# Performance work log

Measured on AMD Instinct MI355X. Metric: run time of the kernel, lower is better.

## Reference

```python
import jax, jax.numpy as jnp
import numpy as np

N, E = 100000, 640000
H, EDGE_D, ATOM_D, RD, L = 128, 10, 25, 64, 4


def _gelu(t):
    return jax.nn.gelu(t, approximate=True)  # tanh approximation, matches torch GELU(approximate='tanh')


def _mlp2(t, w1, b1, w2, b2):
    return _gelu(t @ w1 + b1) @ w2 + b2


def setup_inputs() -> dict:
    key = jax.random.key(0)
    ks = iter(jax.random.split(key, 64))
    s = 0.05
    d = {}
    d['x'] = jax.random.normal(next(ks), (N, ATOM_D), jnp.float32)
    d['edge_index'] = jax.random.randint(next(ks), (2, E), 0, N, jnp.int32)
    d['edge_attr'] = jax.random.normal(next(ks), (E, EDGE_D), jnp.float32)
    d['enc_w1'] = jax.random.normal(next(ks), (ATOM_D, H)) * s
    d['enc_b1'] = jnp.zeros((H,))
    d['enc_w2'] = jax.random.normal(next(ks), (H, H)) * s
    d['enc_b2'] = jnp.zeros((H,))
    d['edge_w1'] = jax.random.normal(next(ks), (L, EDGE_D, H)) * s
    d['edge_b1'] = jnp.zeros((L, H))
    d['edge_w2'] = jax.random.normal(next(ks), (L, H, H)) * s
    d['edge_b2'] = jnp.zeros((L, H))
    d['msg_w1'] = jax.random.normal(next(ks), (L, H, H)) * s
    d['msg_b1'] = jnp.zeros((L, H))
    d['msg_w2'] = jax.random.normal(next(ks), (L, H, H)) * s
    d['msg_b2'] = jnp.zeros((L, H))
    d['gate_w'] = jax.random.normal(next(ks), (L, 2 * H, H)) * s
    d['gate_b'] = jnp.zeros((L, H))
    d['ln_g'] = jnp.ones((L, H))
    d['ln_b'] = jnp.zeros((L, H))
    for name in ('ion', 'pka', 'acid'):
        d[name + '_w1'] = jax.random.normal(next(ks), (H, RD)) * s
        d[name + '_b1'] = jnp.zeros((RD,))
        d[name + '_w2'] = jax.random.normal(next(ks), (RD, 1)) * s
        d[name + '_b2'] = jnp.zeros((1,))
    return d


def reference(x, edge_index, edge_attr, enc_w1, enc_b1, enc_w2, enc_b2,
              edge_w1, edge_b1, edge_w2, edge_b2,
              msg_w1, msg_b1, msg_w2, msg_b2,
              gate_w, gate_b, ln_g, ln_b,
              ion_w1, ion_b1, ion_w2, ion_b2,
              pka_w1, pka_b1, pka_w2, pka_b2,
              acid_w1, acid_b1, acid_w2, acid_b2):
    src, dst = edge_index[0], edge_index[1]
    n = x.shape[0]
    h = _mlp2(x, enc_w1, enc_b1, enc_w2, enc_b2)  # [N, H]
    ones_e = jnp.ones((src.shape[0],), x.dtype)
    count = jnp.clip(jax.ops.segment_sum(ones_e, dst, num_segments=n), 1.0)[:, None]  # [N,1]
    for i in range(L):
        ew = _mlp2(edge_attr, edge_w1[i], edge_b1[i], edge_w2[i], edge_b2[i])  # [E, H]
        msg = _mlp2(h[src], msg_w1[i], msg_b1[i], msg_w2[i], msg_b2[i]) * ew   # [E, H]
        agg = jax.ops.segment_sum(msg, dst, num_segments=n) / count           # [N, H] mean agg
        gate = jax.nn.sigmoid(jnp.concatenate([h, agg], axis=-1) @ gate_w[i] + gate_b[i])
        h = h + gate * agg
        mu = jnp.mean(h, axis=-1, keepdims=True)
        var = jnp.mean(jnp.square(h - mu), axis=-1, keepdims=True)
        h = (h - mu) * jax.lax.rsqrt(var + 1e-5) * ln_g[i] + ln_b[i]
    ion = _mlp2(h, ion_w1, ion_b1, ion_w2, ion_b2)
    pka = _mlp2(h, pka_w1, pka_b1, pka_w2, pka_b2)
    acid = _mlp2(h, acid_w1, acid_b1, acid_w2, acid_b2)
    return (ion, pka, acid)
```

## Files before the change

### kernel.cpp

```cpp
#include <hip/hip_runtime.h>
#include <math.h>

#define NN 100000
#define NN2 100032
#define NE 640000
#define H 128
#define AD 25
#define ED 10
#define RD 64
#define NL 4
#define NB_E (NE / 64 + 1)
#define NSB ((NN + 255) / 256)
#define CAP 256

typedef short bfrag __attribute__((ext_vector_type(8)));
typedef float floatx4 __attribute__((ext_vector_type(4)));
typedef unsigned short ushort;

#define MFMA(a, b, c) __builtin_amdgcn_mfma_f32_16x16x32_bf16(a, b, c, 0, 0, 0)

__device__ __forceinline__ ushort f2bf(float f) {
    unsigned u = __float_as_uint(f);
    unsigned r = (u + 0x7FFFu + ((u >> 16) & 1u)) >> 16;
    return (ushort)r;
}
__device__ __forceinline__ float bf2f(ushort b) {
    return __uint_as_float(((unsigned)b) << 16);
}
__device__ __forceinline__ float gelu_t(float x) {
    float u = 0.7978845608028654f * (x + 0.044715f * x * x * x);
    float e = __expf(2.0f * u);
    float th = 1.0f - 2.0f / (e + 1.0f);
    return 0.5f * x * (1.0f + th);
}
__device__ __forceinline__ float sigm(float x) {
    return 1.0f / (1.0f + __expf(-x));
}

__global__ void k_wt(const float* __restrict__ src, ushort* __restrict__ dst,
                     int Ks, int N, int Kd, int total) {
    for (int idx = blockIdx.x * 256 + threadIdx.x; idx < total; idx += gridDim.x * 256) {
        int nk = N * Kd;
        int b = idx / nk;
        int rem = idx - b * nk;
        int n = rem / Kd, k = rem - n * Kd;
        float v = (k < Ks) ? src[((size_t)b * Ks + k) * N + n] : 0.0f;
        dst[idx] = f2bf(v);
    }
}
__global__ void k_cvt(const float* __restrict__ src, ushort* __restrict__ dst,
                      int rs, int Ks, int Kd, int total) {
    for (int idx = blockIdx.x * 256 + threadIdx.x; idx < total; idx += gridDim.x * 256) {
        int r = idx / Kd, k = idx - r * Kd;
        dst[idx] = (r < rs && k < Ks) ? f2bf(src[(size_t)r * Ks + k]) : 0;
    }
}
__global__ void k_cvtperm(const float* __restrict__ ea, const int* __restrict__ perm,
                          ushort* __restrict__ out) {
    int j = blockIdx.x * 256 + threadIdx.x;
    if (j >= NE) return;
    const float* src = ea + (size_t)perm[j] * ED;
    unsigned u[8];
#pragma unroll
    for (int k = 0; k < 5; ++k)
        u[k] = (unsigned)f2bf(src[2 * k]) | ((unsigned)f2bf(src[2 * k + 1]) << 16);
    u[5] = u[6] = u[7] = 0u;
    uint4* o = (uint4*)(out + (size_t)j * 16);
    uint4 a; a.x = u[0]; a.y = u[1]; a.z = u[2]; a.w = u[3];
    uint4 b; b.x = u[4]; b.y = u[5]; b.z = u[6]; b.w = u[7];
    o[0] = a; o[1] = b;
}

__global__ void k_hist(const int* __restrict__ ei, int* __restrict__ hist) {
    int e = blockIdx.x * 256 + threadIdx.x;
    if (e < NE) atomicAdd(&hist[ei[NE + e]], 1);
}
__global__ void k_scan1(const int* __restrict__ hist, int* __restrict__ incl,
                        int* __restrict__ bsum) {
    __shared__ int s[256];
    int tid = threadIdx.x;
    int i = blockIdx.x * 256 + tid;
    s[tid] = (i < NN) ? hist[i] : 0;
    __syncthreads();
    for (int off = 1; off < 256; off <<= 1) {
        int t = (tid >= off) ? s[tid - off] : 0;
        __syncthreads();
        s[tid] += t;
        __syncthreads();
    }
    if (i < NN) incl[i] = s[tid];
    if (tid == 255) bsum[blockIdx.x] = s[255];
}
__global__ void k_scan2(int* __restrict__ bsum) {
    __shared__ int s[512];
    int tid = threadIdx.x;
    s[tid] = (tid < NSB) ? bsum[tid] : 0;
    __syncthreads();
    for (int off = 1; off < 512; off <<= 1) {
        int t = (tid >= off) ? s[tid - off] : 0;
        __syncthreads();
        s[tid] += t;
        __syncthreads();
    }
    if (tid < NSB) bsum[tid] = (tid > 0) ? s[tid - 1] : 0;
}
__global__ void k_scan3(const int* __restrict__ hist, const int* __restrict__ incl,
                        const int* __restrict__ bsum, int* __restrict__ row_ptr) {
    int i = blockIdx.x * 256 + threadIdx.x;
    if (i < NN) row_ptr[i] = bsum[blockIdx.x] + incl[i] - hist[i];
    if (i == 0) row_ptr[NN] = NE;
}
__global__ void k_scatter(const int* __restrict__ ei, int* __restrict__ cursor,
                          int* __restrict__ perm) {
    int e = blockIdx.x * 256 + threadIdx.x;
    if (e < NE) {
        int d = ei[NE + e];
        int pos = atomicAdd(&cursor[d], 1);
        perm[pos] = e;
    }
}
__global__ void k_blockrange(const int* __restrict__ row_ptr, int* __restrict__ nf,
                             int* __restrict__ nl) {
    int n = blockIdx.x * 256 + threadIdx.x;
    if (n < NN) {
        int b = row_ptr[n] >> 6;
        atomicMin(&nf[b], n);
        atomicMax(&nl[b], n);
    }
}

template <int K1>
__global__ void __launch_bounds__(256)
k_mlp2mf(const ushort* __restrict__ Abf, ushort* __restrict__ Obf,
         const ushort* __restrict__ W1t, const float* __restrict__ B1,
         const ushort* __restrict__ W2t, const float* __restrict__ B2) {
    __shared__ ushort sH[64 * 136];
    const int tid = threadIdx.x;
    const int w = tid >> 6, lane = tid & 63, lr = lane & 15, lg = lane >> 4;
    const int rowB = blockIdx.x * 64 + w * 16 + lr;

    floatx4 acc[8];
#pragma unroll
    for (int t = 0; t < 8; ++t) acc[t] = (floatx4){0.f, 0.f, 0.f, 0.f};
#pragma unroll
    for (int kb = 0; kb < K1 / 32; ++kb) {
        bfrag bv = *(const bfrag*)(Abf + (size_t)rowB * K1 + kb * 32 + lg * 8);
#pragma unroll
        for (int t = 0; t < 8; ++t) {
            bfrag av = *(const bfrag*)(W1t + (t * 16 + lr) * K1 + kb * 32 + lg * 8);
            acc[t] = MFMA(av, bv, acc[t]);
        }
    }
    ushort* sHrow = sH + (w * 16 + lr) * 136;
#pragma unroll
    for (int t = 0; t < 8; ++t) {
        const float4 b1 = *(const float4*)(B1 + t * 16 + lg * 4);
        float h0 = gelu_t(acc[t][0] + b1.x), h1 = gelu_t(acc[t][1] + b1.y);
        float h2 = gelu_t(acc[t][2] + b1.z), h3 = gelu_t(acc[t][3] + b1.w);
        uint2 p;
        p.x = (unsigned)f2bf(h0) | ((unsigned)f2bf(h1) << 16);
        p.y = (unsigned)f2bf(h2) | ((unsigned)f2bf(h3) << 16);
        *(uint2*)(sHrow + t * 16 + lg * 4) = p;
    }
#pragma unroll
    for (int t = 0; t < 8; ++t) acc[t] = (floatx4){0.f, 0.f, 0.f, 0.f};
#pragma unroll
    for (int kb = 0; kb < 4; ++kb) {
        bfrag av = *(const bfrag*)(sH + (w * 16 + lr) * 136 + kb * 32 + lg * 8);
#pragma unroll
        for (int t = 0; t < 8; ++t) {
            bfrag bv = *(const bfrag*)(W2t + (t * 16 + lr) * 128 + kb * 32 + lg * 8);
            acc[t] = MFMA(av, bv, acc[t]);
        }
    }
    const int rowD = blockIdx.x * 64 + w * 16 + lg * 4;
#pragma unroll
    for (int t = 0; t < 8; ++t) {
        const int col = t * 16 + lr;
        const float b2 = B2[col];
#pragma unroll
        for (int r = 0; r < 4; ++r) {
            int row = rowD + r;
            if (row < NN) Obf[(size_t)row * 128 + col] = f2bf(acc[t][r] + b2);
        }
    }
}

__global__ void __launch_bounds__(256)
k_ew(const ushort* __restrict__ eap, ushort* __restrict__ ewp, int S,
     const ushort* __restrict__ W1t, const float* __restrict__ B1,
     const ushort* __restrict__ W2t, const float* __restrict__ B2) {
    __shared__ ushort sea[128 * 40];
    __shared__ ushort sH[4][16 * 136];
    const int tid = threadIdx.x;
    const int w = tid >> 6, lane = tid & 63, lr = lane & 15, lg = lane >> 4;
    const int jl0 = blockIdx.x * 128;

    {
        int r = tid >> 1, half = tid & 1;
        int j = S + jl0 + r;
        uint4 z; z.x = z.y = z.z = z.w = 0u;
        uint4 v = z;
        if (j < NE) v = *(const uint4*)(eap + (size_t)j * 16 + half * 8);
        *(uint4*)(sea + r * 40 + half * 8) = v;
        *(uint4*)(sea + r * 40 + 16 + half * 8) = z;
    }
    __syncthreads();

    for (int rt = 0; rt < 2; ++rt) {
        const int row_l = w * 32 + rt * 16;
        floatx4 acc[8];
#pragma unroll
        for (int t = 0; t < 8; ++t) acc[t] = (floatx4){0.f, 0.f, 0.f, 0.f};
        bfrag bv = *(const bfrag*)(sea + (row_l + lr) * 40 + lg * 8);
#pragma unroll
        for (int t = 0; t < 8; ++t) {
            bfrag av = *(const bfrag*)(W1t + (t * 16 + lr) * 32 + lg * 8);
            acc[t] = MFMA(av, bv, acc[t]);
        }
        ushort* sHr = sH[w] + lr * 136;
#pragma unroll
        for (int t = 0; t < 8; ++t) {
            const float4 b1 = *(const float4*)(B1 + t * 16 + lg * 4);
            float h0 = gelu_t(acc[t][0] + b1.x), h1 = gelu_t(acc[t][1] + b1.y);
            float h2 = gelu_t(acc[t][2] + b1.z), h3 = gelu_t(acc[t][3] + b1.w);
            uint2 p;
            p.x = (unsigned)f2bf(h0) | ((unsigned)f2bf(h1) << 16);
            p.y = (unsigned)f2bf(h2) | ((unsigned)f2bf(h3) << 16);
            *(uint2*)(sHr + t * 16 + lg * 4) = p;
        }
#pragma unroll
        for (int t = 0; t < 8; ++t) acc[t] = (floatx4){0.f, 0.f, 0.f, 0.f};
#pragma unroll
        for (int kb = 0; kb < 4; ++kb) {
            bfrag av = *(const bfrag*)(sH[w] + lr * 136 + kb * 32 + lg * 8);
#pragma unroll
            for (int t = 0; t < 8; ++t) {
                bfrag bw = *(const bfrag*)(W2t + (t * 16 + lr) * 128 + kb * 32 + lg * 8);
                acc[t] = MFMA(bw, av, acc[t]);
            }
        }
        const int jl = jl0 + row_l + lr;
        if (S + jl < NE) {
            ushort* orow = ewp + (size_t)jl * 128;
#pragma unroll
            for (int t = 0; t < 8; ++t) {
                const float4 b2 = *(const float4*)(B2 + t * 16 + lg * 4);
                uint2 p;
                p.x = (unsigned)f2bf(acc[t][0] + b2.x) |
                      ((unsigned)f2bf(acc[t][1] + b2.y) << 16);
                p.y = (unsigned)f2bf(acc[t][2] + b2.z) |
                      ((unsigned)f2bf(acc[t][3] + b2.w) << 16);
                *(uint2*)(orow + t * 16 + lg * 4) = p;
            }
        }
    }
}

__global__ void __launch_bounds__(256)
k_gms(const int* __restrict__ ei, const int* __restrict__ perm,
      const int* __restrict__ row_ptr, const int* __restrict__ nf,
      const int* __restrict__ nl, const ushort* __restrict__ ewp, int S,
      const ushort* __restrict__ mbf, ushort* __restrict__ aggbf) {
    __shared__ int ssrc[CAP], sdst[CAP], sseg[CAP];
    __shared__ int snode[64];
    __shared__ float sinvd[64];
    __shared__ float sagg[64 * 132];
    __shared__ int swtot[4];
    __shared__ int s_nseg;

    const int b = blockIdx.x;
    const int n0 = nf[b];
    if (n0 >= NN) return;
    const int n1 = nl[b];
    const int e0 = row_ptr[n0];
    int ne = row_ptr[n1 + 1] - e0;
    if (ne <= 0) return;
    const int ncl = (ne < CAP) ? ne : CAP;

    const int tid = threadIdx.x;
    const int w = tid >> 6, lane = tid & 63;

    for (int i = tid; i < 64 * 132; i += 256) sagg[i] = 0.0f;

    int dstv = -1 - tid;
    if (tid < ncl) {
        int e = perm[e0 + tid];
        ssrc[tid] = ei[e];
        dstv = ei[NE + e];
    }
    sdst[tid] = dstv;
    __syncthreads();

    int f = 0;
    if (tid < ncl) f = (tid == 0) ? 1 : (sdst[tid] != sdst[tid - 1]);
    unsigned long long mk = __ballot(f);
    int incl = __popcll(mk & (~0ull >> (63 - lane)));
    if (lane == 63) swtot[w] = incl;
    __syncthreads();
    int woff = 0;
    for (int i = 0; i < w; ++i) woff += swtot[i];
    int segid = woff + incl;
    sseg[tid] = segid - 1;
    if (f) {
        int s = segid - 1;
        snode[s] = dstv;
        sinvd[s] = 1.0f / (float)(row_ptr[dstv + 1] - row_ptr[dstv]);
    }
    if (tid == 255) s_nseg = segid;
    __syncthreads();
    const int nseg = s_nseg;

    const int c0 = (tid & 31) * 4;
    const int g = tid >> 5;
    const int chunk = (ncl + 7) >> 3;
    const int j0 = g * chunk;
    const int j1 = (j0 + chunk < ncl) ? (j0 + chunk) : ncl;
    const int be = e0 - S;
    int cs = -1;
    float v0 = 0.f, v1 = 0.f, v2 = 0.f, v3 = 0.f;
    for (int j = j0; j < j1; ++j) {
        uint2 ew = *(const uint2*)(ewp + (size_t)(be + j) * 128 + c0);
        uint2 mv = *(const uint2*)(mbf + (size_t)ssrc[j] * 128 + c0);
        float a0 = bf2f((ushort)(ew.x & 0xFFFF)) * bf2f((ushort)(mv.x & 0xFFFF));
        float a1 = bf2f((ushort)(ew.x >> 16)) * bf2f((ushort)(mv.x >> 16));
        float a2 = bf2f((ushort)(ew.y & 0xFFFF)) * bf2f((ushort)(mv.y & 0xFFFF));
        float a3 = bf2f((ushort)(ew.y >> 16)) * bf2f((ushort)(mv.y >> 16));
        int sg = sseg[j];
        if (sg != cs) {
            if (cs >= 0) {
                float* p = &sagg[cs * 132 + c0];
                atomicAdd(p + 0, v0); atomicAdd(p + 1, v1);
                atomicAdd(p + 2, v2); atomicAdd(p + 3, v3);
            }
            cs = sg; v0 = a0; v1 = a1; v2 = a2; v3 = a3;
        } else {
            v0 += a0; v1 += a1; v2 += a2; v3 += a3;
        }
    }
    if (cs >= 0) {
        float* p = &sagg[cs * 132 + c0];
        atomicAdd(p + 0, v0); atomicAdd(p + 1, v1);
        atomicAdd(p + 2, v2); atomicAdd(p + 3, v3);
    }
    __syncthreads();
    for (int i = tid; i < nseg * 32; i += 256) {
        int s = i >> 5, qd = i & 31;
        float inv = sinvd[s];
        const float* p = &sagg[s * 132 + qd * 4];
        uint2 pk;
        pk.x = (unsigned)f2bf(p[0] * inv) | ((unsigned)f2bf(p[1] * inv) << 16);
        pk.y = (unsigned)f2bf(p[2] * inv) | ((unsigned)f2bf(p[3] * inv) << 16);
        *(uint2*)(aggbf + (size_t)snode[s] * 128 + qd * 4) = pk;
    }
}

template <int WITH_MSG>
__global__ void __launch_bounds__(256)
k_gatemlp(ushort* __restrict__ hbf, const ushort* __restrict__ aggbf,
          const ushort* __restrict__ GWt, const float* __restrict__ GB,
          const float* __restrict__ LNG, const float* __restrict__ LNB,
          const ushort* __restrict__ W1t, const float* __restrict__ B1,
          const ushort* __restrict__ W2t, const float* __restrict__ B2,
          ushort* __restrict__ mbf) {
    __shared__ ushort sA[64 * 136];
    const int tid = threadIdx.x;
    const int w = tid >> 6, lane = tid & 63, lr = lane & 15, lg = lane >> 4;
    const int row = blockIdx.x * 64 + w * 16 + lr;

    floatx4 acc[8];
#pragma unroll
    for (int t = 0; t < 8; ++t) acc[t] = (floatx4){0.f, 0.f, 0.f, 0.f};
#pragma unroll
    for (int kb = 0; kb < 8; ++kb) {
        bfrag bv;
        if (kb < 4) bv = *(const bfrag*)(hbf + (size_t)row * 128 + kb * 32 + lg * 8);
        else bv = *(const bfrag*)(aggbf + (size_t)row * 128 + (kb - 4) * 32 + lg * 8);
#pragma unroll
        for (int t = 0; t < 8; ++t) {
            bfrag av = *(const bfrag*)(GWt + (t * 16 + lr) * 256 + kb * 32 + lg * 8);
            acc[t] = MFMA(av, bv, acc[t]);
        }
    }
    float o[8][4];
    float s = 0.0f;
#pragma unroll
    for (int t = 0; t < 8; ++t) {
        const int c0 = t * 16 + lg * 4;
        const float4 gb = *(const float4*)(GB + c0);
        uint2 hp = *(const uint2*)(hbf + (size_t)row * 128 + c0);
        uint2 ap = *(const uint2*)(aggbf + (size_t)row * 128 + c0);
        float h0 = bf2f((ushort)(hp.x & 0xFFFF)), h1 = bf2f((ushort)(hp.x >> 16));
        float h2 = bf2f((ushort)(hp.y & 0xFFFF)), h3 = bf2f((ushort)(hp.y >> 16));
        float a0 = bf2f((ushort)(ap.x & 0xFFFF)), a1 = bf2f((ushort)(ap.x >> 16));
        float a2 = bf2f((ushort)(ap.y & 0xFFFF)), a3 = bf2f((ushort)(ap.y >> 16));
        o[t][0] = h0 + sigm(acc[t][0] + gb.x) * a0;
        o[t][1] = h1 + sigm(acc[t][1] + gb.y) * a1;
        o[t][2] = h2 + sigm(acc[t][2] + gb.z) * a2;
        o[t][3] = h3 + sigm(acc[t][3] + gb.w) * a3;
        s += o[t][0] + o[t][1] + o[t][2] + o[t][3];
    }
    s += __shfl_xor(s, 16);
    s += __shfl_xor(s, 32);
    const float mu = s * (1.0f / 128.0f);
    float q = 0.0f;
#pragma unroll
    for (int t = 0; t < 8; ++t)
#pragma unroll
        for (int r = 0; r < 4; ++r) {
            float dx = o[t][r] - mu;
            q = fmaf(dx, dx, q);
        }
    q += __shfl_xor(q, 16);
    q += __shfl_xor(q, 32);
    const float rs = rsqrtf(q * (1.0f / 128.0f) + 1e-5f);

    ushort* sArow = sA + (w * 16 + lr) * 136;
#pragma unroll
    for (int t = 0; t < 8; ++t) {
        const int c0 = t * 16 + lg * 4;
        const float4 g4 = *(const float4*)(LNG + c0);
        const float4 b4 = *(const float4*)(LNB + c0);
        float r0 = fmaf((o[t][0] - mu) * rs, g4.x, b4.x);
        float r1 = fmaf((o[t][1] - mu) * rs, g4.y, b4.y);
        float r2 = fmaf((o[t][2] - mu) * rs, g4.z, b4.z);
        float r3 = fmaf((o[t][3] - mu) * rs, g4.w, b4.w);
        uint2 pk;
        pk.x = (unsigned)f2bf(r0) | ((unsigned)f2bf(r1) << 16);
        pk.y = (unsigned)f2bf(r2) | ((unsigned)f2bf(r3) << 16);
        if (row < NN) *(uint2*)(hbf + (size_t)row * 128 + c0) = pk;
        if (WITH_MSG) *(uint2*)(sArow + c0) = pk;
    }

    if (WITH_MSG) {
#pragma unroll
        for (int t = 0; t < 8; ++t) acc[t] = (floatx4){0.f, 0.f, 0.f, 0.f};
#pragma unroll
        for (int kb = 0; kb < 4; ++kb) {
            bfrag bv = *(const bfrag*)(sA + (w * 16 + lr) * 136 + kb * 32 + lg * 8);
#pragma unroll
            for (int t = 0; t < 8; ++t) {
                bfrag av = *(const bfrag*)(W1t + (t * 16 + lr) * 128 + kb * 32 + lg * 8);
                acc[t] = MFMA(av, bv, acc[t]);
            }
        }
#pragma unroll
        for (int t = 0; t < 8; ++t) {
            const float4 b1 = *(const float4*)(B1 + t * 16 + lg * 4);
            float h0 = gelu_t(acc[t][0] + b1.x), h1 = gelu_t(acc[t][1] + b1.y);
            float h2 = gelu_t(acc[t][2] + b1.z), h3 = gelu_t(acc[t][3] + b1.w);
            uint2 p;
            p.x = (unsigned)f2bf(h0) | ((unsigned)f2bf(h1) << 16);
            p.y = (unsigned)f2bf(h2) | ((unsigned)f2bf(h3) << 16);
            *(uint2*)(sArow + t * 16 + lg * 4) = p;
        }
#pragma unroll
        for (int t = 0; t < 8; ++t) acc[t] = (floatx4){0.f, 0.f, 0.f, 0.f};
#pragma unroll
        for (int kb = 0; kb < 4; ++kb) {
            bfrag av = *(const bfrag*)(sA + (w * 16 + lr) * 136 + kb * 32 + lg * 8);
#pragma unroll
            for (int t = 0; t < 8; ++t) {
                bfrag bv = *(const bfrag*)(W2t + (t * 16 + lr) * 128 + kb * 32 + lg * 8);
                acc[t] = MFMA(av, bv, acc[t]);
            }
        }
        const int rowD = blockIdx.x * 64 + w * 16 + lg * 4;
#pragma unroll
        for (int t = 0; t < 8; ++t) {
            const int col = t * 16 + lr;
            const float b2 = B2[col];
#pragma unroll
            for (int r = 0; r < 4; ++r) {
                int rw = rowD + r;
                if (rw < NN) mbf[(size_t)rw * 128 + col] = f2bf(acc[t][r] + b2);
            }
        }
    }
}

__global__ void __launch_bounds__(256)
k_headsmf(const ushort* __restrict__ hbf, float* __restrict__ OUT,
          const ushort* __restrict__ WHt,
          const float* __restrict__ b1a, const float* __restrict__ b1b, const float* __restrict__ b1c,
          const float* __restrict__ w2a, const float* __restrict__ w2b, const float* __restrict__ w2c,
          const float* __restrict__ b2a, const float* __restrict__ b2b, const float* __restrict__ b2c) {
    const int tid = threadIdx.x;
    const int w = tid >> 6, lane = tid & 63, lr = lane & 15, lg = lane >> 4;
    const int row = blockIdx.x * 64 + w * 16 + lr;

    floatx4 acc[12];
#pragma unroll
    for (int t = 0; t < 12; ++t) acc[t] = (floatx4){0.f, 0.f, 0.f, 0.f};
#pragma unroll
    for (int kb = 0; kb < 4; ++kb) {
        bfrag bv = *(const bfrag*)(hbf + (size_t)row * 128 + kb * 32 + lg * 8);
#pragma unroll
        for (int t = 0; t < 12; ++t) {
            bfrag av = *(const bfrag*)(WHt + (t * 16 + lr) * 128 + kb * 32 + lg * 8);
            acc[t] = MFMA(av, bv, acc[t]);
        }
    }
    const float* b1s[3] = {b1a, b1b, b1c};
    const float* w2s[3] = {w2a, w2b, w2c};
    float p[3] = {0.f, 0.f, 0.f};
#pragma unroll
    for (int t = 0; t < 12; ++t) {
        const int head = t >> 2;
        const int c0 = (t & 3) * 16 + lg * 4;
        const float4 b1 = *(const float4*)(b1s[head] + c0);
        const float4 w2 = *(const float4*)(w2s[head] + c0);
        p[head] += gelu_t(acc[t][0] + b1.x) * w2.x;
        p[head] += gelu_t(acc[t][1] + b1.y) * w2.y;
        p[head] += gelu_t(acc[t][2] + b1.z) * w2.z;
        p[head] += gelu_t(acc[t][3] + b1.w) * w2.w;
    }
#pragma unroll
    for (int hd = 0; hd < 3; ++hd) {
        p[hd] += __shfl_xor(p[hd], 16);
        p[hd] += __shfl_xor(p[hd], 32);
    }
    if (lg == 0 && row < NN) {
        OUT[0 * NN + row] = p[0] + b2a[0];
        OUT[1 * NN + row] = p[1] + b2b[0];
        OUT[2 * NN + row] = p[2] + b2c[0];
    }
}

extern "C" void kernel_launch(void* const* d_in, const int* in_sizes, int n_in,
                              void* d_out, int out_size, void* d_ws, size_t ws_size,
                              hipStream_t stream) {
    const float* x       = (const float*)d_in[0];
    const int*   ei      = (const int*)d_in[1];
    const float* ea      = (const float*)d_in[2];
    const float* enc_w1  = (const float*)d_in[3];
    const float* enc_b1  = (const float*)d_in[4];
    const float* enc_w2  = (const float*)d_in[5];
    const float* enc_b2  = (const float*)d_in[6];
    const float* edge_w1 = (const float*)d_in[7];
    const float* edge_b1 = (const float*)d_in[8];
    const float* edge_w2 = (const float*)d_in[9];
    const float* edge_b2 = (const float*)d_in[10];
    const float* msg_w1  = (const float*)d_in[11];
    const float* msg_b1  = (const float*)d_in[12];
    const float* msg_w2  = (const float*)d_in[13];
    const float* msg_b2  = (const float*)d_in[14];
    const float* gate_w  = (const float*)d_in[15];
    const float* gate_b  = (const float*)d_in[16];
    const float* ln_g    = (const float*)d_in[17];
    const float* ln_b    = (const float*)d_in[18];
    const float* hw[12];
    for (int t = 0; t < 12; ++t) hw[t] = (const float*)d_in[19 + t];

    const size_t NNH = (size_t)NN2 * H;
    ushort* hbf   = (ushort*)d_ws;
    ushort* mbf   = hbf + NNH;
    ushort* aggbf = mbf + NNH;
    ushort* xbf   = aggbf + NNH;
    ushort* eapbf = xbf + (size_t)NN2 * 32;
    ushort* wt    = eapbf + (size_t)NE * 16;
    ushort* wt_enc1 = wt;
    ushort* wt_enc2 = wt_enc1 + 128 * 32;
    ushort* wt_e1   = wt_enc2 + 128 * 128;
    ushort* wt_e2   = wt_e1 + 4 * 128 * 32;
    ushort* wt_m1   = wt_e2 + 4 * 128 * 128;
    ushort* wt_m2   = wt_m1 + 4 * 128 * 128;
    ushort* wt_g    = wt_m2 + 4 * 128 * 128;
    ushort* wt_h    = wt_g + 4 * 128 * 256;
    int* row_ptr = (int*)(wt_h + 192 * 128 + 64);
    int* perm    = row_ptr + 100352;
    int* nf      = perm + NE;
    int* nl      = nf + 10240;
    int* hist    = nl + 10240;
    int* incl    = hist + 100352;
    int* cursor  = incl + 100352;
    int* bsum    = cursor + 100352;
    uintptr_t ewp_addr = ((uintptr_t)(bsum + 512) + 15) & ~(uintptr_t)15;
    ushort* ewp = (ushort*)ewp_addr;
    const size_t used = ewp_addr - (uintptr_t)d_ws;

    int P = 4;
    size_t rows = NE / 4 + 1024;
    if (ws_size >= used + (size_t)NE * 128 * 2) { P = 1; rows = NE; }
    else if (ws_size >= used + ((size_t)NE / 2 + 1024) * 128 * 2) { P = 2; rows = NE / 2 + 1024; }
    const int PE = NE / P;
    const int NGB = 10000 / P;
    const int ewblk = (int)(rows / 128);

    hipMemsetAsync(hist, 0, NN * sizeof(int), stream);
    hipMemsetAsync(nf, 0x7f, NB_E * sizeof(int), stream);
    hipMemsetAsync(nl, 0xff, NB_E * sizeof(int), stream);
    hipMemsetAsync(aggbf, 0, NNH * sizeof(ushort), stream);
    k_hist<<<(NE + 255) / 256, 256, 0, stream>>>(ei, hist);
    k_scan1<<<NSB, 256, 0, stream>>>(hist, incl, bsum);
    k_scan2<<<1, 512, 0, stream>>>(bsum);
    k_scan3<<<NSB, 256, 0, stream>>>(hist, incl, bsum, row_ptr);
    hipMemcpyAsync(cursor, row_ptr, NN * sizeof(int), hipMemcpyDeviceToDevice, stream);
    k_scatter<<<(NE + 255) / 256, 256, 0, stream>>>(ei, cursor, perm);
    k_blockrange<<<(NN + 255) / 256, 256, 0, stream>>>(row_ptr, nf, nl);

    k_wt<<<64, 256, 0, stream>>>(enc_w1, wt_enc1, 25, 128, 32, 128 * 32);
    k_wt<<<64, 256, 0, stream>>>(enc_w2, wt_enc2, 128, 128, 128, 128 * 128);
    k_wt<<<64, 256, 0, stream>>>(edge_w1, wt_e1, 10, 128, 32, 4 * 128 * 32);
    k_wt<<<256, 256, 0, stream>>>(edge_w2, wt_e2, 128, 128, 128, 4 * 128 * 128);
    k_wt<<<256, 256, 0, stream>>>(msg_w1, wt_m1, 128, 128, 128, 4 * 128 * 128);
    k_wt<<<256, 256, 0, stream>>>(msg_w2, wt_m2, 128, 128, 128, 4 * 128 * 128);
    k_wt<<<512, 256, 0, stream>>>(gate_w, wt_g, 256, 128, 256, 4 * 128 * 256);
    k_wt<<<32, 256, 0, stream>>>(hw[0], wt_h, 128, 64, 128, 64 * 128);
    k_wt<<<32, 256, 0, stream>>>(hw[4], wt_h + 64 * 128, 128, 64, 128, 64 * 128);
    k_wt<<<32, 256, 0, stream>>>(hw[8], wt_h + 128 * 128, 128, 64, 128, 64 * 128);
    k_cvt<<<3200, 256, 0, stream>>>(x, xbf, NN, 25, 32, NN2 * 32);
    k_cvtperm<<<(NE + 255) / 256, 256, 0, stream>>>(ea, perm, eapbf);

    const int ntiles = NN2 / 64;
    k_mlp2mf<32><<<ntiles, 256, 0, stream>>>(xbf, hbf,
        wt_enc1, enc_b1, wt_enc2, enc_b2);
    k_mlp2mf<128><<<ntiles, 256, 0, stream>>>(hbf, mbf,
        wt_m1, msg_b1, wt_m2, msg_b2);

    for (int l = 0; l < NL; ++l) {
        for (int p = 0; p < P; ++p) {
            const int S = p * PE;
            k_ew<<<ewblk, 256, 0, stream>>>(eapbf, ewp, S,
                wt_e1 + (size_t)l * 128 * 32, edge_b1 + l * H,
                wt_e2 + (size_t)l * 128 * 128, edge_b2 + l * H);
            const int nb = (p == P - 1) ? (NGB + 1) : NGB;
            k_gms<<<nb, 256, 0, stream>>>(ei, perm, row_ptr,
                nf + p * NGB, nl + p * NGB, ewp, S, mbf, aggbf);
        }
        if (l < NL - 1) {
            k_gatemlp<1><<<ntiles, 256, 0, stream>>>(hbf, aggbf,
                wt_g + (size_t)l * 128 * 256, gate_b + l * H,
                ln_g + l * H, ln_b + l * H,
                wt_m1 + (size_t)(l + 1) * 128 * 128, msg_b1 + (l + 1) * H,
                wt_m2 + (size_t)(l + 1) * 128 * 128, msg_b2 + (l + 1) * H, mbf);
        } else {
            k_gatemlp<0><<<ntiles, 256, 0, stream>>>(hbf, aggbf,
                wt_g + (size_t)l * 128 * 256, gate_b + l * H,
                ln_g + l * H, ln_b + l * H,
                nullptr, nullptr, nullptr, nullptr, nullptr);
        }
    }

    k_headsmf<<<ntiles, 256, 0, stream>>>(hbf, (float*)d_out, wt_h,
        hw[1], hw[5], hw[9], hw[2], hw[6], hw[10], hw[3], hw[7], hw[11]);
}
```

Baseline: 2.272 ms.

## Merge weight conversion launches and hoist operand loads ahead of MFMA loops

```diff
diff --git a/kernel.cpp b/kernel.cpp
--- a/kernel.cpp
+++ b/kernel.cpp
@@ -37,17 +37,35 @@
     return 1.0f / (1.0f + __expf(-x));
 }
 
-__global__ void k_wt(const float* __restrict__ src, ushort* __restrict__ dst,
-                     int Ks, int N, int Kd, int total) {
-    for (int idx = blockIdx.x * 256 + threadIdx.x; idx < total; idx += gridDim.x * 256) {
-        int nk = N * Kd;
-        int b = idx / nk;
-        int rem = idx - b * nk;
-        int n = rem / Kd, k = rem - n * Kd;
-        float v = (k < Ks) ? src[((size_t)b * Ks + k) * N + n] : 0.0f;
-        dst[idx] = f2bf(v);
-    }
-}
+__global__ void k_wtall(ushort* __restrict__ wt,
+                        const float* __restrict__ s0, const float* __restrict__ s1,
+                        const float* __restrict__ s2, const float* __restrict__ s3,
+                        const float* __restrict__ s4, const float* __restrict__ s5,
+                        const float* __restrict__ s6, const float* __restrict__ s7,
+                        const float* __restrict__ s8, const float* __restrict__ s9) {
+    int idx = blockIdx.x * 256 + threadIdx.x;
+    const float* src;
+    int Ks, N, Kd, off;
+    if (idx < 4096)        { src = s0; Ks = 25;  N = 128; Kd = 32;  off = 0; }
+    else if (idx < 20480)  { src = s1; Ks = 128; N = 128; Kd = 128; off = 4096; }
+    else if (idx < 36864)  { src = s2; Ks = 10;  N = 128; Kd = 32;  off = 20480; }
+    else if (idx < 102400) { src = s3; Ks = 128; N = 128; Kd = 128; off = 36864; }
+    else if (idx < 167936) { src = s4; Ks = 128; N = 128; Kd = 128; off = 102400; }
+    else if (idx < 233472) { src = s5; Ks = 128; N = 128; Kd = 128; off = 167936; }
+    else if (idx < 364544) { src = s6; Ks = 256; N = 128; Kd = 256; off = 233472; }
+    else if (idx < 372736) { src = s7; Ks = 128; N = 64;  Kd = 128; off = 364544; }
+    else if (idx < 380928) { src = s8; Ks = 128; N = 64;  Kd = 128; off = 372736; }
+    else if (idx < 389120) { src = s9; Ks = 128; N = 64;  Kd = 128; off = 380928; }
+    else return;
+    int lidx = idx - off;
+    int nk = N * Kd;
+    int b = lidx / nk;
+    int rem = lidx - b * nk;
+    int n = rem / Kd, k = rem - n * Kd;
+    float v = (k < Ks) ? src[((size_t)b * Ks + k) * N + n] : 0.0f;
+    wt[idx] = f2bf(v);
+}
+
 __global__ void k_cvt(const float* __restrict__ src, ushort* __restrict__ dst,
                       int rs, int Ks, int Kd, int total) {
     for (int idx = blockIdx.x * 256 + threadIdx.x; idx < total; idx += gridDim.x * 256) {
@@ -139,16 +157,20 @@
     const int w = tid >> 6, lane = tid & 63, lr = lane & 15, lg = lane >> 4;
     const int rowB = blockIdx.x * 64 + w * 16 + lr;
 
+    bfrag bvv[K1 / 32];
+#pragma unroll
+    for (int kb = 0; kb < K1 / 32; ++kb)
+        bvv[kb] = *(const bfrag*)(Abf + (size_t)rowB * K1 + kb * 32 + lg * 8);
+
     floatx4 acc[8];
 #pragma unroll
     for (int t = 0; t < 8; ++t) acc[t] = (floatx4){0.f, 0.f, 0.f, 0.f};
 #pragma unroll
     for (int kb = 0; kb < K1 / 32; ++kb) {
-        bfrag bv = *(const bfrag*)(Abf + (size_t)rowB * K1 + kb * 32 + lg * 8);
 #pragma unroll
         for (int t = 0; t < 8; ++t) {
             bfrag av = *(const bfrag*)(W1t + (t * 16 + lr) * K1 + kb * 32 + lg * 8);
-            acc[t] = MFMA(av, bv, acc[t]);
+            acc[t] = MFMA(av, bvv[kb], acc[t]);
         }
     }
     ushort* sHrow = sH + (w * 16 + lr) * 136;
@@ -205,6 +227,10 @@
         *(uint4*)(sea + r * 40 + half * 8) = v;
         *(uint4*)(sea + r * 40 + 16 + half * 8) = z;
     }
+    bfrag av1[8];
+#pragma unroll
+    for (int t = 0; t < 8; ++t)
+        av1[t] = *(const bfrag*)(W1t + (t * 16 + lr) * 32 + lg * 8);
     __syncthreads();
 
     for (int rt = 0; rt < 2; ++rt) {
@@ -214,10 +240,7 @@
         for (int t = 0; t < 8; ++t) acc[t] = (floatx4){0.f, 0.f, 0.f, 0.f};
         bfrag bv = *(const bfrag*)(sea + (row_l + lr) * 40 + lg * 8);
 #pragma unroll
-        for (int t = 0; t < 8; ++t) {
-            bfrag av = *(const bfrag*)(W1t + (t * 16 + lr) * 32 + lg * 8);
-            acc[t] = MFMA(av, bv, acc[t]);
-        }
+        for (int t = 0; t < 8; ++t) acc[t] = MFMA(av1[t], bv, acc[t]);
         ushort* sHr = sH[w] + lr * 136;
 #pragma unroll
         for (int t = 0; t < 8; ++t) {
@@ -319,13 +342,21 @@
     const int be = e0 - S;
     int cs = -1;
     float v0 = 0.f, v1 = 0.f, v2 = 0.f, v3 = 0.f;
+    uint2 ewc, mvc;
+    if (j0 < j1) {
+        ewc = *(const uint2*)(ewp + (size_t)(be + j0) * 128 + c0);
+        mvc = *(const uint2*)(mbf + (size_t)ssrc[j0] * 128 + c0);
+    }
     for (int j = j0; j < j1; ++j) {
-        uint2 ew = *(const uint2*)(ewp + (size_t)(be + j) * 128 + c0);
-        uint2 mv = *(const uint2*)(mbf + (size_t)ssrc[j] * 128 + c0);
-        float a0 = bf2f((ushort)(ew.x & 0xFFFF)) * bf2f((ushort)(mv.x & 0xFFFF));
-        float a1 = bf2f((ushort)(ew.x >> 16)) * bf2f((ushort)(mv.x >> 16));
-        float a2 = bf2f((ushort)(ew.y & 0xFFFF)) * bf2f((ushort)(mv.y & 0xFFFF));
-        float a3 = bf2f((ushort)(ew.y >> 16)) * bf2f((ushort)(mv.y >> 16));
+        uint2 ewn = ewc, mvn = mvc;
+        if (j + 1 < j1) {
+            ewn = *(const uint2*)(ewp + (size_t)(be + j + 1) * 128 + c0);
+            mvn = *(const uint2*)(mbf + (size_t)ssrc[j + 1] * 128 + c0);
+        }
+        float a0 = bf2f((ushort)(ewc.x & 0xFFFF)) * bf2f((ushort)(mvc.x & 0xFFFF));
+        float a1 = bf2f((ushort)(ewc.x >> 16)) * bf2f((ushort)(mvc.x >> 16));
+        float a2 = bf2f((ushort)(ewc.y & 0xFFFF)) * bf2f((ushort)(mvc.y & 0xFFFF));
+        float a3 = bf2f((ushort)(ewc.y >> 16)) * bf2f((ushort)(mvc.y >> 16));
         int sg = sseg[j];
         if (sg != cs) {
             if (cs >= 0) {
@@ -337,6 +368,7 @@
         } else {
             v0 += a0; v1 += a1; v2 += a2; v3 += a3;
         }
+        ewc = ewn; mvc = mvn;
     }
     if (cs >= 0) {
         float* p = &sagg[cs * 132 + c0];
@@ -368,18 +400,29 @@
     const int w = tid >> 6, lane = tid & 63, lr = lane & 15, lg = lane >> 4;
     const int row = blockIdx.x * 64 + w * 16 + lr;
 
+    bfrag bvv[8];
+    uint2 hp[8], ap[8];
+#pragma unroll
+    for (int kb = 0; kb < 4; ++kb)
+        bvv[kb] = *(const bfrag*)(hbf + (size_t)row * 128 + kb * 32 + lg * 8);
+#pragma unroll
+    for (int kb = 0; kb < 4; ++kb)
+        bvv[4 + kb] = *(const bfrag*)(aggbf + (size_t)row * 128 + kb * 32 + lg * 8);
+#pragma unroll
+    for (int t = 0; t < 8; ++t) {
+        hp[t] = *(const uint2*)(hbf + (size_t)row * 128 + t * 16 + lg * 4);
+        ap[t] = *(const uint2*)(aggbf + (size_t)row * 128 + t * 16 + lg * 4);
+    }
+
     floatx4 acc[8];
 #pragma unroll
     for (int t = 0; t < 8; ++t) acc[t] = (floatx4){0.f, 0.f, 0.f, 0.f};
 #pragma unroll
     for (int kb = 0; kb < 8; ++kb) {
-        bfrag bv;
-        if (kb < 4) bv = *(const bfrag*)(hbf + (size_t)row * 128 + kb * 32 + lg * 8);
-        else bv = *(const bfrag*)(aggbf + (size_t)row * 128 + (kb - 4) * 32 + lg * 8);
 #pragma unroll
         for (int t = 0; t < 8; ++t) {
             bfrag av = *(const bfrag*)(GWt + (t * 16 + lr) * 256 + kb * 32 + lg * 8);
-            acc[t] = MFMA(av, bv, acc[t]);
+            acc[t] = MFMA(av, bvv[kb], acc[t]);
         }
     }
     float o[8][4];
@@ -388,12 +431,10 @@
     for (int t = 0; t < 8; ++t) {
         const int c0 = t * 16 + lg * 4;
         const float4 gb = *(const float4*)(GB + c0);
-        uint2 hp = *(const uint2*)(hbf + (size_t)row * 128 + c0);
-        uint2 ap = *(const uint2*)(aggbf + (size_t)row * 128 + c0);
-        float h0 = bf2f((ushort)(hp.x & 0xFFFF)), h1 = bf2f((ushort)(hp.x >> 16));
-        float h2 = bf2f((ushort)(hp.y & 0xFFFF)), h3 = bf2f((ushort)(hp.y >> 16));
-        float a0 = bf2f((ushort)(ap.x & 0xFFFF)), a1 = bf2f((ushort)(ap.x >> 16));
-        float a2 = bf2f((ushort)(ap.y & 0xFFFF)), a3 = bf2f((ushort)(ap.y >> 16));
+        float h0 = bf2f((ushort)(hp[t].x & 0xFFFF)), h1 = bf2f((ushort)(hp[t].x >> 16));
+        float h2 = bf2f((ushort)(hp[t].y & 0xFFFF)), h3 = bf2f((ushort)(hp[t].y >> 16));
+        float a0 = bf2f((ushort)(ap[t].x & 0xFFFF)), a1 = bf2f((ushort)(ap[t].x >> 16));
+        float a2 = bf2f((ushort)(ap[t].y & 0xFFFF)), a3 = bf2f((ushort)(ap[t].y >> 16));
         o[t][0] = h0 + sigm(acc[t][0] + gb.x) * a0;
         o[t][1] = h1 + sigm(acc[t][1] + gb.y) * a1;
         o[t][2] = h2 + sigm(acc[t][2] + gb.z) * a2;
@@ -492,13 +533,16 @@
     floatx4 acc[12];
 #pragma unroll
     for (int t = 0; t < 12; ++t) acc[t] = (floatx4){0.f, 0.f, 0.f, 0.f};
+    bfrag bvv[4];
+#pragma unroll
+    for (int kb = 0; kb < 4; ++kb)
+        bvv[kb] = *(const bfrag*)(hbf + (size_t)row * 128 + kb * 32 + lg * 8);
 #pragma unroll
     for (int kb = 0; kb < 4; ++kb) {
-        bfrag bv = *(const bfrag*)(hbf + (size_t)row * 128 + kb * 32 + lg * 8);
 #pragma unroll
         for (int t = 0; t < 12; ++t) {
             bfrag av = *(const bfrag*)(WHt + (t * 16 + lr) * 128 + kb * 32 + lg * 8);
-            acc[t] = MFMA(av, bv, acc[t]);
+            acc[t] = MFMA(av, bvv[kb], acc[t]);
         }
     }
     const float* b1s[3] = {b1a, b1b, b1c};
@@ -599,16 +643,8 @@
     k_scatter<<<(NE + 255) / 256, 256, 0, stream>>>(ei, cursor, perm);
     k_blockrange<<<(NN + 255) / 256, 256, 0, stream>>>(row_ptr, nf, nl);
 
-    k_wt<<<64, 256, 0, stream>>>(enc_w1, wt_enc1, 25, 128, 32, 128 * 32);
-    k_wt<<<64, 256, 0, stream>>>(enc_w2, wt_enc2, 128, 128, 128, 128 * 128);
-    k_wt<<<64, 256, 0, stream>>>(edge_w1, wt_e1, 10, 128, 32, 4 * 128 * 32);
-    k_wt<<<256, 256, 0, stream>>>(edge_w2, wt_e2, 128, 128, 128, 4 * 128 * 128);
-    k_wt<<<256, 256, 0, stream>>>(msg_w1, wt_m1, 128, 128, 128, 4 * 128 * 128);
-    k_wt<<<256, 256, 0, stream>>>(msg_w2, wt_m2, 128, 128, 128, 4 * 128 * 128);
-    k_wt<<<512, 256, 0, stream>>>(gate_w, wt_g, 256, 128, 256, 4 * 128 * 256);
-    k_wt<<<32, 256, 0, stream>>>(hw[0], wt_h, 128, 64, 128, 64 * 128);
-    k_wt<<<32, 256, 0, stream>>>(hw[4], wt_h + 64 * 128, 128, 64, 128, 64 * 128);
-    k_wt<<<32, 256, 0, stream>>>(hw[8], wt_h + 128 * 128, 128, 64, 128, 64 * 128);
+    k_wtall<<<1520, 256, 0, stream>>>(wt, enc_w1, enc_w2, edge_w1, edge_w2,
+                                      msg_w1, msg_w2, gate_w, hw[0], hw[4], hw[8]);
     k_cvt<<<3200, 256, 0, stream>>>(x, xbf, NN, 25, 32, NN2 * 32);
     k_cvtperm<<<(NE + 255) / 256, 256, 0, stream>>>(ea, perm, eapbf);
 
```

After: 2.230 ms. About the same (-1.9%).
